# Kernel optimization log

Measured on AMD Instinct MI355X. Metric: run time of the kernel, lower is better.

## Reference

```python
import jax, jax.numpy as jnp
import numpy as np

D_MODEL = 1024
NUM_HEADS = 16
HEAD_DIM = D_MODEL // NUM_HEADS


def setup_inputs() -> dict:
    key = jax.random.key(0)
    ks = jax.random.split(key, 11)
    B, S = 2, 2048
    inp = {
        "query": jax.random.normal(ks[0], (B, S, D_MODEL), jnp.float32),
        "key": jax.random.normal(ks[1], (B, S, D_MODEL), jnp.float32),
        "value": jax.random.normal(ks[2], (B, S, D_MODEL), jnp.float32),
        "mask": 1,
        "w_q": jax.random.normal(ks[3], (D_MODEL, D_MODEL), jnp.float32) / np.sqrt(D_MODEL),
        "b_q": jax.random.normal(ks[4], (D_MODEL,), jnp.float32) * 0.02,
        "w_k": jax.random.normal(ks[5], (D_MODEL, D_MODEL), jnp.float32) / np.sqrt(D_MODEL),
        "b_k": jax.random.normal(ks[6], (D_MODEL,), jnp.float32) * 0.02,
        "w_v": jax.random.normal(ks[7], (D_MODEL, D_MODEL), jnp.float32) / np.sqrt(D_MODEL),
        "b_v": jax.random.normal(ks[8], (D_MODEL,), jnp.float32) * 0.02,
        "w_o": jax.random.normal(ks[9], (D_MODEL, D_MODEL), jnp.float32) / np.sqrt(D_MODEL),
        "b_o": jax.random.normal(ks[10], (D_MODEL,), jnp.float32) * 0.02,
    }
    return inp


def reference(query, key, value, mask, w_q, b_q, w_k, b_k, w_v, b_v, w_o, b_o):
    B, S, _ = query.shape
    H, Dh = NUM_HEADS, HEAD_DIM
    # projections (torch Linear: x @ W.T + b; here w_* stored as [in, out])
    q = (query @ w_q + b_q).reshape(B, S, H, Dh).transpose(0, 2, 1, 3)  # [B,H,S,Dh]
    k = (key @ w_k + b_k).reshape(B, S, H, Dh).transpose(0, 2, 1, 3)
    v = (value @ w_v + b_v).reshape(B, S, H, Dh).transpose(0, 2, 1, 3)
    scale = 1.0 / jnp.sqrt(jnp.asarray(Dh, q.dtype))
    scores = jnp.einsum("bhqd,bhkd->bhqk", q, k) * scale  # [B,H,S,S]
    if mask:
        causal = jnp.tril(jnp.ones((S, S), dtype=bool))
        scores = jnp.where(causal, scores, jnp.asarray(-1e9, scores.dtype))
    attn = jax.nn.softmax(scores, axis=-1)
    x = jnp.einsum("bhqk,bhkd->bhqd", attn, v)  # [B,H,S,Dh]
    x = x.transpose(0, 2, 1, 3).reshape(B, S, H * Dh)
    return x @ w_o + b_o
```

## Files before the change

### kernel.cpp

```cpp
#include <hip/hip_runtime.h>
#include <hip/hip_bf16.h>

using bf16 = __hip_bfloat16;

typedef __attribute__((ext_vector_type(4))) short short4v;
typedef __attribute__((ext_vector_type(8))) short short8v;
typedef __attribute__((ext_vector_type(4))) float f32x4;

static constexpr int D  = 1024;
static constexpr int H  = 16;
static constexpr int DH = 64;
static constexpr int B  = 2;
static constexpr int S  = 2048;
static constexpr int M  = B * S;
static constexpr size_t MD = (size_t)M * D;
static constexpr size_t WSZ = (size_t)D * D;

#define QS_CONST 0.18033688011112042f

__device__ __forceinline__ unsigned short f2b(float f) {
    union { float f; unsigned u; } v; v.f = f;
    return (unsigned short)((v.u + 0x7FFFu + ((v.u >> 16) & 1u)) >> 16);
}
__device__ __forceinline__ unsigned pkbf(float a, float b) {
    float2 t; t.x = a; t.y = b;
    __hip_bfloat162 h = __float22bfloat162_rn(t);
    union { __hip_bfloat162 h; unsigned u; } cv; cv.h = h;
    return cv.u;
}
__device__ __forceinline__ short8v pack8(short4v a, short4v b) {
    short8v r;
    r[0]=a[0]; r[1]=a[1]; r[2]=a[2]; r[3]=a[3];
    r[4]=b[0]; r[5]=b[1]; r[6]=b[2]; r[7]=b[3];
    return r;
}
__device__ __forceinline__ short8v ld_frag(const short* rowp, int lg) {
    short4v a = *reinterpret_cast<const short4v*>(rowp + 4*lg);
    short4v b = *reinterpret_cast<const short4v*>(rowp + 16 + 4*lg);
    return pack8(a, b);
}

__device__ __forceinline__ void gl_lds16(const void* g, void* l) {
    __builtin_amdgcn_global_load_lds(
        (const __attribute__((address_space(1))) unsigned int*)g,
        (__attribute__((address_space(3))) unsigned int*)l, 16, 0, 0);
}

__global__ __launch_bounds__(256) void cvt_all_kernel(
    const float* __restrict__ w0, const float* __restrict__ w1,
    const float* __restrict__ w2, const float* __restrict__ w3,
    unsigned short* __restrict__ t0, unsigned short* __restrict__ t1,
    unsigned short* __restrict__ t2, unsigned short* __restrict__ t3,
    const float* __restrict__ x0, const float* __restrict__ x1,
    const float* __restrict__ x2,
    unsigned short* __restrict__ y0, unsigned short* __restrict__ y1,
    unsigned short* __restrict__ y2)
{
    __shared__ float tile[32][33];
    const int z = blockIdx.z;
    if (z < 4) {
        const float* W = z==0 ? w0 : z==1 ? w1 : z==2 ? w2 : w3;
        unsigned short* T = z==0 ? t0 : z==1 ? t1 : z==2 ? t2 : t3;
        const int k0 = (blockIdx.x & 31) * 32, n0 = (blockIdx.x >> 5) * 32;
        const int t = threadIdx.x, r = t>>3, c4 = (t&7)*4;
        float4 v = *reinterpret_cast<const float4*>(&W[(size_t)(k0+r)*D + n0 + c4]);
        tile[r][c4+0]=v.x; tile[r][c4+1]=v.y; tile[r][c4+2]=v.z; tile[r][c4+3]=v.w;
        __syncthreads();
        uint2 p;
        p.x = pkbf(tile[c4+0][r], tile[c4+1][r]);
        p.y = pkbf(tile[c4+2][r], tile[c4+3][r]);
        *reinterpret_cast<uint2*>(T + (size_t)(n0+r)*D + k0 + c4) = p;
    } else {
        const float* X = z==4 ? x0 : z==5 ? x1 : x2;
        unsigned short* Y = z==4 ? y0 : z==5 ? y1 : y2;
        const size_t base = (size_t)blockIdx.x * 256 + threadIdx.x;
        const size_t stride = (size_t)1024 * 256;
#pragma unroll
        for (int j = 0; j < 4; ++j) {
            const size_t i = base + (size_t)j * stride;
            float4 f = reinterpret_cast<const float4*>(X)[i];
            uint2 p; p.x = pkbf(f.x, f.y); p.y = pkbf(f.z, f.w);
            reinterpret_cast<uint2*>(Y)[i] = p;
        }
    }
}

#define GEMM_CORE_LDS(XPTR, WPTR)                                              \
    __shared__ short As[2][128*32];                                            \
    __shared__ short Bs[2][128*32];                                            \
    const int tid = threadIdx.x;                                               \
    const int wid = tid>>6, lane = tid&63;                                     \
    const int wr = wid>>1, wc = wid&1;                                         \
    const int lg = lane>>4, lr = lane&15;                                      \
    const int qw = (lane&3) ^ ((lane>>3)&3);        \
    const int qr = lg ^ ((lr>>1)&3);                \
    f32x4 acc[4][4];                                                           \
    _Pragma("unroll")                                                          \
    for (int i=0;i<4;i++)                                                      \
        _Pragma("unroll")                                                      \
        for (int j=0;j<4;j++) acc[i][j] = f32x4{0.f,0.f,0.f,0.f};              \
    const int srow = (lane>>2);                                                \
    auto stage = [&](int buf, int k0) {                                        \
        _Pragma("unroll")                                                      \
        for (int c=0;c<2;c++) {                                                \
            const int r0 = 32*wid + 16*c;                                      \
            const int r  = r0 + srow;                                          \
            gl_lds16(XPTR + (size_t)(m0+r)*1024 + k0 + qw*8, &As[buf][r0*32]); \
            gl_lds16(WPTR + (size_t)(n0+r)*1024 + k0 + qw*8, &Bs[buf][r0*32]); \
        }                                                                      \
    };                                                                         \
    stage(0, 0);                                                               \
    int cur = 0;                                                               \
    for (int k0 = 0; k0 < 1024; k0 += 32) {                                    \
        __syncthreads();                     \
        if (k0 + 32 < 1024) stage(cur^1, k0 + 32);                             \
        short8v af[4], bfr[4];                                                 \
        _Pragma("unroll")                                                      \
        for (int i=0;i<4;i++) {                                                \
            const int R = wr*64 + i*16 + lr;                                   \
            af[i] = *reinterpret_cast<const short8v*>(&As[cur][R*32 + qr*8]);  \
        }                                                                      \
        _Pragma("unroll")                                                      \
        for (int j=0;j<4;j++) {                                                \
            const int R = wc*64 + j*16 + lr;                                   \
            bfr[j] = *reinterpret_cast<const short8v*>(&Bs[cur][R*32 + qr*8]); \
        }                                                                      \
        __builtin_amdgcn_s_setprio(1);                                         \
        _Pragma("unroll")                                                      \
        for (int i=0;i<4;i++)                                                  \
            _Pragma("unroll")                                                  \
            for (int j=0;j<4;j++)                                              \
                acc[i][j] = __builtin_amdgcn_mfma_f32_16x16x32_bf16(           \
                    af[i], bfr[j], acc[i][j], 0,0,0);                          \
        __builtin_amdgcn_s_setprio(0);                                         \
        cur ^= 1;                                                              \
    }

__global__ __launch_bounds__(256) void gemm_qkv_lds(
    const unsigned short* __restrict__ Xq, const unsigned short* __restrict__ Xk,
    const unsigned short* __restrict__ Xv, const unsigned short* __restrict__ WtBase,
    const float* __restrict__ bq, const float* __restrict__ bk,
    const float* __restrict__ bv, unsigned short* __restrict__ qkBase,
    unsigned short* __restrict__ va)
{
    const int z = blockIdx.z;
    const unsigned short* X = z==0 ? Xq : z==1 ? Xk : Xv;
    const unsigned short* Wt = WtBase + (size_t)z * WSZ;
    const float* bias = z==0 ? bq : z==1 ? bk : bv;
    const int m0 = blockIdx.x*128, n0 = blockIdx.y*128;

    GEMM_CORE_LDS(X, Wt)

#pragma unroll
    for (int i=0;i<4;i++) {
#pragma unroll
        for (int j=0;j<4;j++) {
            const int n = n0 + wc*64 + j*16 + lr;
            const float bv2 = bias[n];
#pragma unroll
            for (int r=0;r<4;r++) {
                const int m = m0 + wr*64 + i*16 + lg*4 + r;
                float v = acc[i][j][r] + bv2;
                const int bb=m>>11, ss=m&2047, hh=n>>6, dh=n&63;
                if (z == 0) {
                    v *= QS_CONST;
                    qkBase[(((size_t)(bb*H+hh))*S + ss)*DH + dh] = f2b(v);
                } else if (z == 1) {
                    (qkBase + MD)[(((size_t)(bb*H+hh))*S + ss)*DH + dh] = f2b(v);
                } else {
                    va[(((size_t)(bb*H+hh))*DH + dh)*S + ss] = f2b(v);
                }
            }
        }
    }
}

template<int OUTBF>
__global__ __launch_bounds__(256) void gemm_out_lds(
    const unsigned short* __restrict__ Xc, const unsigned short* __restrict__ Wt,
    const float* __restrict__ bias, void* __restrict__ Y)
{
    const int m0 = blockIdx.x*128, n0 = blockIdx.y*128;

    GEMM_CORE_LDS(Xc, Wt)

#pragma unroll
    for (int i=0;i<4;i++) {
#pragma unroll
        for (int j=0;j<4;j++) {
            const int n = n0 + wc*64 + j*16 + lr;
            const float bv = bias[n];
#pragma unroll
            for (int r=0;r<4;r++) {
                const int m = m0 + wr*64 + i*16 + lg*4 + r;
                const float v = acc[i][j][r] + bv;
                if (OUTBF) ((unsigned short*)Y)[(size_t)m*D + n] = f2b(v);
                else       ((float*)Y)[(size_t)m*D + n] = v;
            }
        }
    }
}

__global__ __launch_bounds__(512) void attn_mfma(
    const unsigned short* __restrict__ Qa,
    const unsigned short* __restrict__ Ka,
    const unsigned short* __restrict__ Va,
    unsigned short* __restrict__ Ctx)
{
    __shared__ short Ks[2][64][72];
    __shared__ short Vs[2][64][72];
    short (*Ob)[72] = (short(*)[72])Ks;

    const int tid = threadIdx.x;
    const int i   = blockIdx.x;
    const int xcd = i & 7;
    const int o   = i >> 3;
    const int bh  = (xcd << 2) + (o >> 4);
    const int qt  = (o < 32) ? (o & 15) : 15 - (o & 15);
    const int bb = bh>>4, hh = bh&15;
    const int q0 = qt*128;
    const int wid = tid>>6, lane = tid&63;
    const int lg = lane>>4, lr = lane&15;
    const size_t qkbase = (size_t)bh*S*DH;
    const size_t vbase  = (size_t)bh*DH*S;

    const int qrow = q0 + wid*16 + lr;
    short8v qf[2];
    {
        const unsigned short* qp = Qa + qkbase + (size_t)qrow*DH;
#pragma unroll
        for (int c=0;c<2;c++) {
            short4v a = *reinterpret_cast<const short4v*>(qp + 32*c + 4*lg);
            short4v b = *reinterpret_cast<const short4v*>(qp + 32*c + 16 + 4*lg);
            qf[c] = pack8(a, b);
        }
    }

    float lsum = 0.f;
    f32x4 oacc[4];
#pragma unroll
    for (int dt=0;dt<4;dt++) oacc[dt] = f32x4{0.f,0.f,0.f,0.f};

    const int sr = tid>>3;
    const int sc = (tid&7)*8;

    uint4 kg, vg;
    auto load_kv = [&](int j0) {
        kg = *reinterpret_cast<const uint4*>(Ka + qkbase + (size_t)(j0+sr)*DH + sc);
        vg = *reinterpret_cast<const uint4*>(Va + vbase  + (size_t)sr*S + j0 + sc);
    };
    auto store_kv = [&](int buf) {
        *reinterpret_cast<uint4*>(&Ks[buf][sr][sc]) = kg;
        *reinterpret_cast<uint4*>(&Vs[buf][sr][sc]) = vg;
    };

    const int NT = 2*qt + 2;
    load_kv(0);
    store_kv(0);

    for (int t = 0; t < NT; ++t) {
        const int j0 = t*64;
        const int cur = t & 1;
        if (t + 1 < NT) load_kv(j0 + 64);
        __syncthreads();

        __builtin_amdgcn_s_setprio(1);
        f32x4 st[4];
#pragma unroll
        for (int jt=0;jt<4;jt++) {
            f32x4 s = f32x4{0.f,0.f,0.f,0.f};
#pragma unroll
            for (int c=0;c<2;c++) {
                short8v kf = ld_frag(&Ks[cur][jt*16 + lr][32*c], lg);
                s = __builtin_amdgcn_mfma_f32_16x16x32_bf16(kf, qf[c], s, 0,0,0);
            }
            st[jt] = s;
        }
        __builtin_amdgcn_s_setprio(0);

        float p[16];
        if (t >= NT-2) {
#pragma unroll
            for (int jt=0;jt<4;jt++)
#pragma unroll
                for (int r=0;r<4;r++) {
                    const int j = j0 + jt*16 + lg*4 + r;
                    p[jt*4+r] = (j <= qrow) ? st[jt][r] : -1e30f;
                }
        } else {
#pragma unroll
            for (int jt=0;jt<4;jt++)
#pragma unroll
                for (int r=0;r<4;r++) p[jt*4+r] = st[jt][r];
        }
#pragma unroll
        for (int e=0;e<16;e++) { p[e] = exp2f(p[e]); lsum += p[e]; }

        uint4 u0, u1;
        u0.x = pkbf(p[0],p[1]);   u0.y = pkbf(p[2],p[3]);
        u0.z = pkbf(p[4],p[5]);   u0.w = pkbf(p[6],p[7]);
        u1.x = pkbf(p[8],p[9]);   u1.y = pkbf(p[10],p[11]);
        u1.z = pkbf(p[12],p[13]); u1.w = pkbf(p[14],p[15]);
        short8v pf0, pf1;
        *reinterpret_cast<uint4*>(&pf0) = u0;
        *reinterpret_cast<uint4*>(&pf1) = u1;

        __builtin_amdgcn_s_setprio(1);
#pragma unroll
        for (int dt=0;dt<4;dt++) {
            short8v vf0 = ld_frag(&Vs[cur][dt*16 + lr][0],  lg);
            short8v vf1 = ld_frag(&Vs[cur][dt*16 + lr][32], lg);
            oacc[dt] = __builtin_amdgcn_mfma_f32_16x16x32_bf16(vf0, pf0, oacc[dt], 0,0,0);
            oacc[dt] = __builtin_amdgcn_mfma_f32_16x16x32_bf16(vf1, pf1, oacc[dt], 0,0,0);
        }
        __builtin_amdgcn_s_setprio(0);

        if (t + 1 < NT) store_kv(cur ^ 1);
    }

    lsum += __shfl_xor(lsum, 16);
    lsum += __shfl_xor(lsum, 32);
    __syncthreads();
    const float inv = 1.f / lsum;
#pragma unroll
    for (int dt=0;dt<4;dt++) {
        uint2 w;
        w.x = pkbf(oacc[dt][0]*inv, oacc[dt][1]*inv);
        w.y = pkbf(oacc[dt][2]*inv, oacc[dt][3]*inv);
        *reinterpret_cast<uint2*>(&Ob[wid*16 + lr][dt*16 + lg*4]) = w;
    }
    __syncthreads();
    const int orow = tid>>2, oc = (tid&3)*16;
    uint4 o1 = *reinterpret_cast<const uint4*>(&Ob[orow][oc]);
    uint4 o2 = *reinterpret_cast<const uint4*>(&Ob[orow][oc+8]);
    unsigned short* dst = Ctx + ((size_t)bb*S + q0 + orow)*D + hh*DH + oc;
    *reinterpret_cast<uint4*>(dst)     = o1;
    *reinterpret_cast<uint4*>(dst + 8) = o2;
}

extern "C" void kernel_launch(void* const* d_in, const int* in_sizes, int n_in,
                              void* d_out, int out_size, void* d_ws, size_t ws_size,
                              hipStream_t stream)
{
    const float* query = (const float*)d_in[0];
    const float* key   = (const float*)d_in[1];
    const float* value = (const float*)d_in[2];
    const float* w_q = (const float*)d_in[4];
    const float* b_q = (const float*)d_in[5];
    const float* w_k = (const float*)d_in[6];
    const float* b_k = (const float*)d_in[7];
    const float* w_v = (const float*)d_in[8];
    const float* b_v = (const float*)d_in[9];
    const float* w_o = (const float*)d_in[10];
    const float* b_o = (const float*)d_in[11];

    bool out_bf16 = true;
    {
        size_t ob = 0;
        if (hipMemPtrGetInfo(d_out, &ob) == hipSuccess &&
            ob >= (size_t)out_size * 3 && ob <= (size_t)out_size * 6)
            out_bf16 = false;
    }

    unsigned short* wtq = (unsigned short*)d_ws;
    unsigned short* wtk = wtq + WSZ;
    unsigned short* wtv = wtk + WSZ;
    unsigned short* wto = wtv + WSZ;
    unsigned short* qa  = wto + WSZ;
    unsigned short* ka  = qa  + MD;
    unsigned short* va  = ka  + MD;
    unsigned short* ctx = va  + MD;
    unsigned short* xq  = ctx + MD;
    unsigned short* xk  = xq  + MD;
    unsigned short* xv  = xk  + MD;

    cvt_all_kernel<<<dim3(1024,1,7), 256, 0, stream>>>(
        w_q, w_k, w_v, w_o, wtq, wtk, wtv, wto,
        query, key, value, xq, xk, xv);

    gemm_qkv_lds<<<dim3(M/128, D/128, 3), 256, 0, stream>>>(
        xq, xk, xv, wtq, b_q, b_k, b_v, qa, va);

    attn_mfma<<<dim3((S/128) * B * H), 512, 0, stream>>>(qa, ka, va, ctx);

    if (out_bf16)
        gemm_out_lds<1><<<dim3(M/128, D/128), 256, 0, stream>>>(ctx, wto, b_o, d_out);
    else
        gemm_out_lds<0><<<dim3(M/128, D/128), 256, 0, stream>>>(ctx, wto, b_o, d_out);
}
```

Measured before the change: 130.3 us.

## Split attention into 64-row query tiles with paired causal work per block

The attention kernel now uses 256-thread blocks, each handling two 64-row query tiles (p and 31-p) in sequence, so every block does an equal amount of causal work. Before, it used 512-thread blocks over 128-row tiles with a reversed ordering. The block count stays at 512. Each thread loads twice as much K/V per tile, and the diagonal mask now applies only to the last tile. This is meant to balance load and let more blocks stay resident, but it reloads K/V for the second tile and adds a sync between the two tiles.

```diff
diff --git a/kernel.cpp b/kernel.cpp
--- a/kernel.cpp
+++ b/kernel.cpp
@@ -201,7 +201,7 @@
     }
 }
 
-__global__ __launch_bounds__(512) void attn_mfma(
+__global__ __launch_bounds__(256) void attn_mfma(
     const unsigned short* __restrict__ Qa,
     const unsigned short* __restrict__ Ka,
     const unsigned short* __restrict__ Va,
@@ -209,133 +209,145 @@
 {
     __shared__ short Ks[2][64][72];
     __shared__ short Vs[2][64][72];
-    short (*Ob)[72] = (short(*)[72])Ks;
+    short (*Ob)[72] = Ks[0];
 
     const int tid = threadIdx.x;
     const int i   = blockIdx.x;
     const int xcd = i & 7;
     const int o   = i >> 3;
     const int bh  = (xcd << 2) + (o >> 4);
-    const int qt  = (o < 32) ? (o & 15) : 15 - (o & 15);
+    const int p   = o & 15;
     const int bb = bh>>4, hh = bh&15;
-    const int q0 = qt*128;
     const int wid = tid>>6, lane = tid&63;
     const int lg = lane>>4, lr = lane&15;
     const size_t qkbase = (size_t)bh*S*DH;
     const size_t vbase  = (size_t)bh*DH*S;
 
-    const int qrow = q0 + wid*16 + lr;
-    short8v qf[2];
-    {
-        const unsigned short* qp = Qa + qkbase + (size_t)qrow*DH;
-#pragma unroll
-        for (int c=0;c<2;c++) {
-            short4v a = *reinterpret_cast<const short4v*>(qp + 32*c + 4*lg);
-            short4v b = *reinterpret_cast<const short4v*>(qp + 32*c + 16 + 4*lg);
-            qf[c] = pack8(a, b);
-        }
-    }
-
-    float lsum = 0.f;
-    f32x4 oacc[4];
-#pragma unroll
-    for (int dt=0;dt<4;dt++) oacc[dt] = f32x4{0.f,0.f,0.f,0.f};
-
-    const int sr = tid>>3;
-    const int sc = (tid&7)*8;
-
-    uint4 kg, vg;
+    const int sr = tid>>2;
+    const int sc = (tid&3)*16;
+
+    uint4 kg0, kg1, vg0, vg1;
     auto load_kv = [&](int j0) {
-        kg = *reinterpret_cast<const uint4*>(Ka + qkbase + (size_t)(j0+sr)*DH + sc);
-        vg = *reinterpret_cast<const uint4*>(Va + vbase  + (size_t)sr*S + j0 + sc);
+        const unsigned short* kp = Ka + qkbase + (size_t)(j0+sr)*DH + sc;
+        kg0 = *reinterpret_cast<const uint4*>(kp);
+        kg1 = *reinterpret_cast<const uint4*>(kp + 8);
+        const unsigned short* vp = Va + vbase + (size_t)sr*S + j0 + sc;
+        vg0 = *reinterpret_cast<const uint4*>(vp);
+        vg1 = *reinterpret_cast<const uint4*>(vp + 8);
     };
     auto store_kv = [&](int buf) {
-        *reinterpret_cast<uint4*>(&Ks[buf][sr][sc]) = kg;
-        *reinterpret_cast<uint4*>(&Vs[buf][sr][sc]) = vg;
+        *reinterpret_cast<uint4*>(&Ks[buf][sr][sc])   = kg0;
+        *reinterpret_cast<uint4*>(&Ks[buf][sr][sc+8]) = kg1;
+        *reinterpret_cast<uint4*>(&Vs[buf][sr][sc])   = vg0;
+        *reinterpret_cast<uint4*>(&Vs[buf][sr][sc+8]) = vg1;
     };
 
-    const int NT = 2*qt + 2;
-    load_kv(0);
-    store_kv(0);
-
-    for (int t = 0; t < NT; ++t) {
-        const int j0 = t*64;
-        const int cur = t & 1;
-        if (t + 1 < NT) load_kv(j0 + 64);
+#pragma unroll 1
+    for (int s = 0; s < 2; ++s) {
+        const int qt = s ? (31 - p) : p;
+        const int q0 = qt*64;
+        const int NT = qt + 1;
+        const int qrow = q0 + wid*16 + lr;
+
+        short8v qf[2];
+        {
+            const unsigned short* qp = Qa + qkbase + (size_t)qrow*DH;
+#pragma unroll
+            for (int c=0;c<2;c++) {
+                short4v a = *reinterpret_cast<const short4v*>(qp + 32*c + 4*lg);
+                short4v b = *reinterpret_cast<const short4v*>(qp + 32*c + 16 + 4*lg);
+                qf[c] = pack8(a, b);
+            }
+        }
+
+        float lsum = 0.f;
+        f32x4 oacc[4];
+#pragma unroll
+        for (int dt=0;dt<4;dt++) oacc[dt] = f32x4{0.f,0.f,0.f,0.f};
+
+        load_kv(0);
+        if (s) __syncthreads();
+        store_kv(0);
+
+        for (int t = 0; t < NT; ++t) {
+            const int j0 = t*64;
+            const int cur = t & 1;
+            if (t + 1 < NT) load_kv(j0 + 64);
+            __syncthreads();
+
+            __builtin_amdgcn_s_setprio(1);
+            f32x4 st[4];
+#pragma unroll
+            for (int jt=0;jt<4;jt++) {
+                f32x4 sv = f32x4{0.f,0.f,0.f,0.f};
+#pragma unroll
+                for (int c=0;c<2;c++) {
+                    short8v kf = ld_frag(&Ks[cur][jt*16 + lr][32*c], lg);
+                    sv = __builtin_amdgcn_mfma_f32_16x16x32_bf16(kf, qf[c], sv, 0,0,0);
+                }
+                st[jt] = sv;
+            }
+            __builtin_amdgcn_s_setprio(0);
+
+            float pv[16];
+            if (t == NT-1) {
+#pragma unroll
+                for (int jt=0;jt<4;jt++)
+#pragma unroll
+                    for (int r=0;r<4;r++) {
+                        const int j = j0 + jt*16 + lg*4 + r;
+                        pv[jt*4+r] = (j <= qrow) ? st[jt][r] : -1e30f;
+                    }
+            } else {
+#pragma unroll
+                for (int jt=0;jt<4;jt++)
+#pragma unroll
+                    for (int r=0;r<4;r++) pv[jt*4+r] = st[jt][r];
+            }
+#pragma unroll
+            for (int e=0;e<16;e++) { pv[e] = exp2f(pv[e]); lsum += pv[e]; }
+
+            uint4 u0, u1;
+            u0.x = pkbf(pv[0],pv[1]);   u0.y = pkbf(pv[2],pv[3]);
+            u0.z = pkbf(pv[4],pv[5]);   u0.w = pkbf(pv[6],pv[7]);
+            u1.x = pkbf(pv[8],pv[9]);   u1.y = pkbf(pv[10],pv[11]);
+            u1.z = pkbf(pv[12],pv[13]); u1.w = pkbf(pv[14],pv[15]);
+            short8v pf0, pf1;
+            *reinterpret_cast<uint4*>(&pf0) = u0;
+            *reinterpret_cast<uint4*>(&pf1) = u1;
+
+            __builtin_amdgcn_s_setprio(1);
+#pragma unroll
+            for (int dt=0;dt<4;dt++) {
+                short8v vf0 = ld_frag(&Vs[cur][dt*16 + lr][0],  lg);
+                short8v vf1 = ld_frag(&Vs[cur][dt*16 + lr][32], lg);
+                oacc[dt] = __builtin_amdgcn_mfma_f32_16x16x32_bf16(vf0, pf0, oacc[dt], 0,0,0);
+                oacc[dt] = __builtin_amdgcn_mfma_f32_16x16x32_bf16(vf1, pf1, oacc[dt], 0,0,0);
+            }
+            __builtin_amdgcn_s_setprio(0);
+
+            if (t + 1 < NT) store_kv(cur ^ 1);
+        }
+
+        lsum += __shfl_xor(lsum, 16);
+        lsum += __shfl_xor(lsum, 32);
         __syncthreads();
-
-        __builtin_amdgcn_s_setprio(1);
-        f32x4 st[4];
-#pragma unroll
-        for (int jt=0;jt<4;jt++) {
-            f32x4 s = f32x4{0.f,0.f,0.f,0.f};
-#pragma unroll
-            for (int c=0;c<2;c++) {
-                short8v kf = ld_frag(&Ks[cur][jt*16 + lr][32*c], lg);
-                s = __builtin_amdgcn_mfma_f32_16x16x32_bf16(kf, qf[c], s, 0,0,0);
-            }
-            st[jt] = s;
-        }
-        __builtin_amdgcn_s_setprio(0);
-
-        float p[16];
-        if (t >= NT-2) {
-#pragma unroll
-            for (int jt=0;jt<4;jt++)
-#pragma unroll
-                for (int r=0;r<4;r++) {
-                    const int j = j0 + jt*16 + lg*4 + r;
-                    p[jt*4+r] = (j <= qrow) ? st[jt][r] : -1e30f;
-                }
-        } else {
-#pragma unroll
-            for (int jt=0;jt<4;jt++)
-#pragma unroll
-                for (int r=0;r<4;r++) p[jt*4+r] = st[jt][r];
-        }
-#pragma unroll
-        for (int e=0;e<16;e++) { p[e] = exp2f(p[e]); lsum += p[e]; }
-
-        uint4 u0, u1;
-        u0.x = pkbf(p[0],p[1]);   u0.y = pkbf(p[2],p[3]);
-        u0.z = pkbf(p[4],p[5]);   u0.w = pkbf(p[6],p[7]);
-        u1.x = pkbf(p[8],p[9]);   u1.y = pkbf(p[10],p[11]);
-        u1.z = pkbf(p[12],p[13]); u1.w = pkbf(p[14],p[15]);
-        short8v pf0, pf1;
-        *reinterpret_cast<uint4*>(&pf0) = u0;
-        *reinterpret_cast<uint4*>(&pf1) = u1;
-
-        __builtin_amdgcn_s_setprio(1);
+        const float inv = 1.f / lsum;
 #pragma unroll
         for (int dt=0;dt<4;dt++) {
-            short8v vf0 = ld_frag(&Vs[cur][dt*16 + lr][0],  lg);
-            short8v vf1 = ld_frag(&Vs[cur][dt*16 + lr][32], lg);
-            oacc[dt] = __builtin_amdgcn_mfma_f32_16x16x32_bf16(vf0, pf0, oacc[dt], 0,0,0);
-            oacc[dt] = __builtin_amdgcn_mfma_f32_16x16x32_bf16(vf1, pf1, oacc[dt], 0,0,0);
-        }
-        __builtin_amdgcn_s_setprio(0);
-
-        if (t + 1 < NT) store_kv(cur ^ 1);
-    }
-
-    lsum += __shfl_xor(lsum, 16);
-    lsum += __shfl_xor(lsum, 32);
-    __syncthreads();
-    const float inv = 1.f / lsum;
-#pragma unroll
-    for (int dt=0;dt<4;dt++) {
-        uint2 w;
-        w.x = pkbf(oacc[dt][0]*inv, oacc[dt][1]*inv);
-        w.y = pkbf(oacc[dt][2]*inv, oacc[dt][3]*inv);
-        *reinterpret_cast<uint2*>(&Ob[wid*16 + lr][dt*16 + lg*4]) = w;
-    }
-    __syncthreads();
-    const int orow = tid>>2, oc = (tid&3)*16;
-    uint4 o1 = *reinterpret_cast<const uint4*>(&Ob[orow][oc]);
-    uint4 o2 = *reinterpret_cast<const uint4*>(&Ob[orow][oc+8]);
-    unsigned short* dst = Ctx + ((size_t)bb*S + q0 + orow)*D + hh*DH + oc;
-    *reinterpret_cast<uint4*>(dst)     = o1;
-    *reinterpret_cast<uint4*>(dst + 8) = o2;
+            uint2 w;
+            w.x = pkbf(oacc[dt][0]*inv, oacc[dt][1]*inv);
+            w.y = pkbf(oacc[dt][2]*inv, oacc[dt][3]*inv);
+            *reinterpret_cast<uint2*>(&Ob[wid*16 + lr][dt*16 + lg*4]) = w;
+        }
+        __syncthreads();
+        const int orow = tid>>2, oc = (tid&3)*16;
+        uint4 o1 = *reinterpret_cast<const uint4*>(&Ob[orow][oc]);
+        uint4 o2 = *reinterpret_cast<const uint4*>(&Ob[orow][oc+8]);
+        unsigned short* dst = Ctx + ((size_t)bb*S + q0 + orow)*D + hh*DH + oc;
+        *reinterpret_cast<uint4*>(dst)     = o1;
+        *reinterpret_cast<uint4*>(dst + 8) = o2;
+    }
 }
 
 extern "C" void kernel_launch(void* const* d_in, const int* in_sizes, int n_in,
@@ -381,7 +393,7 @@
     gemm_qkv_lds<<<dim3(M/128, D/128, 3), 256, 0, stream>>>(
         xq, xk, xv, wtq, b_q, b_k, b_v, qa, va);
 
-    attn_mfma<<<dim3((S/128) * B * H), 512, 0, stream>>>(qa, ka, va, ctx);
+    attn_mfma<<<dim3(512), 256, 0, stream>>>(qa, ka, va, ctx);
 
     if (out_bf16)
         gemm_out_lds<1><<<dim3(M/128, D/128), 256, 0, stream>>>(ctx, wto, b_o, d_out);
```

New measurement: 129.3 us. About the same (-0.8%).
